# Optimization experiments

Measured on AMD Instinct MI355X. Metric: run time of the kernel, lower is better.

The kernel has to match this reference:

```python
import jax, jax.numpy as jnp
import numpy as np

B, C_HIGH, C_LOW, H, W = 4, 256, 128, 64, 64
HEADS = 4
HEAD_DIM = C_LOW // HEADS
FFN = 2 * C_LOW
EPS = 1e-5


def group_norm1(x, w, b):
    # GroupNorm(num_groups=1): normalize over (C,H,W) per sample, per-channel affine
    mu = jnp.mean(x, axis=(1, 2, 3), keepdims=True)
    var = jnp.var(x, axis=(1, 2, 3), keepdims=True)
    xn = (x - mu) * jax.lax.rsqrt(var + EPS)
    return xn * w[None, :, None, None] + b[None, :, None, None]


def conv1x1(x, Wm):
    # 1x1 conv, no bias: Wm [C_out, C_in], x [B,C_in,H,W]
    return jnp.einsum('oc,bchw->bohw', Wm, x)


def setup_inputs() -> dict:
    key = jax.random.key(0)
    ks = jax.random.split(key, 10)
    s = 0.05
    return {
        'high_feature': jax.random.normal(ks[0], (B, C_HIGH, H, W), jnp.float32),
        'low_feature': jax.random.normal(ks[1], (B, C_LOW, H, W), jnp.float32),
        'norm_high_w': jnp.ones((C_HIGH,), jnp.float32),
        'norm_high_b': jnp.zeros((C_HIGH,), jnp.float32),
        'norm_low_w': jnp.ones((C_LOW,), jnp.float32),
        'norm_low_b': jnp.zeros((C_LOW,), jnp.float32),
        'norm_ffn_w': jnp.ones((C_LOW,), jnp.float32),
        'norm_ffn_b': jnp.zeros((C_LOW,), jnp.float32),
        'Wq': jax.random.normal(ks[2], (C_LOW, C_HIGH), jnp.float32) * s,
        'Wk': jax.random.normal(ks[3], (C_LOW, C_LOW), jnp.float32) * s,
        'Wv': jax.random.normal(ks[4], (C_LOW, C_LOW), jnp.float32) * s,
        'Wproj': jax.random.normal(ks[5], (C_LOW, C_LOW), jnp.float32) * s,
        'Wffn1': jax.random.normal(ks[6], (FFN, C_LOW), jnp.float32) * s,
        'Wffn2': jax.random.normal(ks[7], (C_LOW, FFN), jnp.float32) * s,
        # nn.Parameter(torch.zeros(1)) in the original; use 0.1 for nontrivial grads
        'gamma_attn': jnp.full((1,), 0.1, jnp.float32),
        'gamma_ffn': jnp.full((1,), 0.1, jnp.float32),
    }


def reference(high_feature, low_feature, norm_high_w, norm_high_b, norm_low_w,
              norm_low_b, norm_ffn_w, norm_ffn_b, Wq, Wk, Wv, Wproj, Wffn1,
              Wffn2, gamma_attn, gamma_ffn):
    Bb, _, Hh, Ww = low_feature.shape
    N = Hh * Ww
    scale = HEAD_DIM ** (-0.5)

    high_norm = group_norm1(high_feature, norm_high_w, norm_high_b)
    low_norm = group_norm1(low_feature, norm_low_w, norm_low_b)

    q = conv1x1(high_norm, Wq).reshape(Bb, HEADS, HEAD_DIM, N).transpose(0, 1, 3, 2)  # [B,h,N,d]
    k = conv1x1(low_norm, Wk).reshape(Bb, HEADS, HEAD_DIM, N)                         # [B,h,d,N]
    v = conv1x1(low_norm, Wv).reshape(Bb, HEADS, HEAD_DIM, N).transpose(0, 1, 3, 2)   # [B,h,N,d]

    attn = jax.nn.softmax(jnp.einsum('bhnd,bhdm->bhnm', q, k) * scale, axis=-1)       # [B,h,N,N]
    out = jnp.einsum('bhnm,bhmd->bhnd', attn, v)                                      # [B,h,N,d]
    out = out.transpose(0, 1, 3, 2).reshape(Bb, C_LOW, Hh, Ww)
    out = conv1x1(out, Wproj)

    x = low_feature + gamma_attn[0] * out
    xn = group_norm1(x, norm_ffn_w, norm_ffn_b)
    ffn = conv1x1(jax.nn.gelu(conv1x1(xn, Wffn1), approximate=False), Wffn2)
    return x + gamma_ffn[0] * ffn
```

## Files before the change

kernel.cpp:

```cpp
#include <hip/hip_runtime.h>
#include <hip/hip_bf16.h>
#include <math.h>

#define EPS 1e-5f
#define BB 4
#define CHIGH 256
#define CLOW 128
#define NN 4096
#define NHEADS 4
#define HDIM 32
#define FFN_DIM 256
#define SPLITS 4

typedef __bf16 b8 __attribute__((ext_vector_type(8)));
typedef float f4 __attribute__((ext_vector_type(4)));

__device__ __forceinline__ unsigned int cvt_pk(float lo, float hi) {
    float2 t; t.x = lo; t.y = hi;
    __hip_bfloat162 h = __float22bfloat162_rn(t);
    unsigned int r;
    __builtin_memcpy(&r, &h, sizeof(r));
    return r;
}
__device__ __forceinline__ float b2f(unsigned short u) {
    unsigned int x = ((unsigned int)u) << 16;
    float f;
    __builtin_memcpy(&f, &x, 4);
    return f;
}
__device__ __forceinline__ float fexp2(float x) {
#if __has_builtin(__builtin_amdgcn_exp2f)
    return __builtin_amdgcn_exp2f(x);
#else
    return exp2f(x);
#endif
}

__global__ __launch_bounds__(256)
void prep_kernel(const float* __restrict__ high, const float* __restrict__ low,
                 float* __restrict__ acc,
                 const float* __restrict__ w0, const float* __restrict__ w1,
                 const float* __restrict__ w2, const float* __restrict__ w3,
                 const float* __restrict__ w4, const float* __restrict__ w5,
                 unsigned short* __restrict__ dst)
{
    const int z = blockIdx.z;
    if (z < 2) {
        const int perSample = z == 0 ? CHIGH * NN : CLOW * NN;
        const float* X = z == 0 ? high : low;
        float* ac = acc + (z == 0 ? 0 : 8);
        const int b = blockIdx.y;
        const float4* xp = (const float4*)(X + (size_t)b * perSample);
        const int n4 = perSample >> 2;
        float s = 0.f, s2 = 0.f;
        for (int i = blockIdx.x * blockDim.x + threadIdx.x; i < n4;
             i += gridDim.x * blockDim.x) {
            float4 v = xp[i];
            s  += v.x + v.y + v.z + v.w;
            s2 += v.x * v.x + v.y * v.y + v.z * v.z + v.w * v.w;
        }
        for (int off = 32; off; off >>= 1) {
            s  += __shfl_down(s, off, 64);
            s2 += __shfl_down(s2, off, 64);
        }
        __shared__ float ls[4], ls2[4];
        const int w = threadIdx.x >> 6;
        if ((threadIdx.x & 63) == 0) { ls[w] = s; ls2[w] = s2; }
        __syncthreads();
        if (threadIdx.x == 0) {
            atomicAdd(&ac[2 * b], ls[0] + ls[1] + ls[2] + ls[3]);
            atomicAdd(&ac[2 * b + 1], ls2[0] + ls2[1] + ls2[2] + ls2[3]);
        }
    } else {
        const int idx = blockIdx.y * 64 + blockIdx.x;
        const int m = idx >> 5;
        if (m >= 6) return;
        const int sizes[6] = {32768, 16384, 16384, 16384, 32768, 32768};
        const int offs[6]  = {0, 32768, 49152, 65536, 81920, 114688};
        const int Ks[6]    = {256, 128, 128, 128, 128, 256};
        const float* src = m == 0 ? w0 : m == 1 ? w1 : m == 2 ? w2 : m == 3 ? w3
                         : m == 4 ? w4 : w5;
        const int i = ((idx & 31) * 256 + threadIdx.x) * 4;
        if (i >= sizes[m]) return;
        const int K = Ks[m];
        const int row = i / K, col = i % K;
        const int mt = row >> 4, mr = row & 15;
        const int kt = col >> 5, kr = col & 31;
        float4 v = *(const float4*)&src[i];
        uint2 pk;
        pk.x = cvt_pk(v.x, v.y);
        pk.y = cvt_pk(v.z, v.w);
        const int doff = offs[m] + (((mt * (K >> 5)) + kt) << 9) + (mr << 5) + kr;
        *(uint2*)&dst[doff] = pk;
    }
}

__global__ __launch_bounds__(256)
void qkv_kernel(const unsigned short* __restrict__ wbf,
                const float* __restrict__ high, const float* __restrict__ low,
                unsigned short* __restrict__ Qt, unsigned short* __restrict__ Kt,
                unsigned short* __restrict__ Vt,
                const float* __restrict__ nh_w, const float* __restrict__ nh_b,
                const float* __restrict__ nl_w, const float* __restrict__ nl_b,
                const float* __restrict__ st)
{
    __shared__ unsigned short XsRaw[32 * 264];
    const int b = blockIdx.y;
    const int n0 = blockIdx.x * 32;
    const int t = threadIdx.x;
    const int w = t >> 6, lm = t & 15, quad = (t & 63) >> 4;
    const int fo = lm * 32 + quad * 8;
    unsigned int* xw = (unsigned int*)XsRaw;

    if (blockIdx.z == 0) {
        const float invCnt = 1.0f / ((float)CHIGH * NN);
        const float mean = st[2 * b] * invCnt;
        const float rstd = rsqrtf(st[2 * b + 1] * invCnt - mean * mean + EPS);
        const float* Xb = high + (size_t)b * CHIGH * NN;
        #pragma unroll
        for (int it = 0; it < 4; it++) {
            const int s = it * 256 + t;
            const int kp = s >> 3;
            const int k2 = kp << 1;
            const int nc = (s & 7) << 2;
            const size_t ro = (size_t)k2 * NN + n0 + nc;
            float4 pa = *(const float4*)&Xb[ro];
            float4 pb = *(const float4*)&Xb[ro + NN];
            const float sc0 = nh_w[k2] * rstd,     sb0 = nh_b[k2] - mean * sc0;
            const float sc1 = nh_w[k2 + 1] * rstd, sb1 = nh_b[k2 + 1] - mean * sc1;
            pa.x = pa.x * sc0 + sb0; pa.y = pa.y * sc0 + sb0;
            pa.z = pa.z * sc0 + sb0; pa.w = pa.w * sc0 + sb0;
            pb.x = pb.x * sc1 + sb1; pb.y = pb.y * sc1 + sb1;
            pb.z = pb.z * sc1 + sb1; pb.w = pb.w * sc1 + sb1;
            xw[(nc + 0) * 132 + kp] = cvt_pk(pa.x, pb.x);
            xw[(nc + 1) * 132 + kp] = cvt_pk(pa.y, pb.y);
            xw[(nc + 2) * 132 + kp] = cvt_pk(pa.z, pb.z);
            xw[(nc + 3) * 132 + kp] = cvt_pk(pa.w, pb.w);
        }
        __syncthreads();
        const int ng = w & 1, mh = w >> 1;
        f4 acc[4];
        #pragma unroll
        for (int f = 0; f < 4; f++) acc[f] = (f4){0.f, 0.f, 0.f, 0.f};
        #pragma unroll
        for (int kc = 0; kc < 8; kc++) {
            b8 bx = *(const b8*)&XsRaw[(ng * 16 + lm) * 264 + kc * 32 + quad * 8];
            #pragma unroll
            for (int f = 0; f < 4; f++) {
                b8 af = *(const b8*)&wbf[(((mh * 4 + f) * 8 + kc) << 9) + fo];
                acc[f] = __builtin_amdgcn_mfma_f32_16x16x32_bf16(af, bx, acc[f], 0, 0, 0);
            }
        }
        const int n = n0 + ng * 16 + lm;
        const float oscale = 0.25503480f;
        #pragma unroll
        for (int f = 0; f < 4; f++) {
            const int mb = mh * 64 + f * 16 + quad * 4;
            const int hh = mb >> 5, ddb = mb & 31;
            uint2 pk;
            pk.x = cvt_pk(acc[f][0] * oscale, acc[f][1] * oscale);
            pk.y = cvt_pk(acc[f][2] * oscale, acc[f][3] * oscale);
            *(uint2*)&Qt[((size_t)(b * NHEADS + hh) * NN + n) * 32 + ddb] = pk;
        }
    } else {
        const unsigned short* Wb = wbf + 32768;
        const float invCnt = 1.0f / ((float)CLOW * NN);
        const float mean = st[8 + 2 * b] * invCnt;
        const float rstd = rsqrtf(st[8 + 2 * b + 1] * invCnt - mean * mean + EPS);
        const float* Xb = low + (size_t)b * CLOW * NN;
        #pragma unroll
        for (int it = 0; it < 2; it++) {
            const int s = it * 256 + t;
            const int kp = s >> 3;
            const int k2 = kp << 1;
            const int nc = (s & 7) << 2;
            const size_t ro = (size_t)k2 * NN + n0 + nc;
            float4 pa = *(const float4*)&Xb[ro];
            float4 pb = *(const float4*)&Xb[ro + NN];
            const float sc0 = nl_w[k2] * rstd,     sb0 = nl_b[k2] - mean * sc0;
            const float sc1 = nl_w[k2 + 1] * rstd, sb1 = nl_b[k2 + 1] - mean * sc1;
            pa.x = pa.x * sc0 + sb0; pa.y = pa.y * sc0 + sb0;
            pa.z = pa.z * sc0 + sb0; pa.w = pa.w * sc0 + sb0;
            pb.x = pb.x * sc1 + sb1; pb.y = pb.y * sc1 + sb1;
            pb.z = pb.z * sc1 + sb1; pb.w = pb.w * sc1 + sb1;
            xw[(nc + 0) * 68 + kp] = cvt_pk(pa.x, pb.x);
            xw[(nc + 1) * 68 + kp] = cvt_pk(pa.y, pb.y);
            xw[(nc + 2) * 68 + kp] = cvt_pk(pa.z, pb.z);
            xw[(nc + 3) * 68 + kp] = cvt_pk(pa.w, pb.w);
        }
        __syncthreads();
        f4 acc[2][4];
        #pragma unroll
        for (int ng = 0; ng < 2; ng++)
            #pragma unroll
            for (int f = 0; f < 4; f++) acc[ng][f] = (f4){0.f, 0.f, 0.f, 0.f};
        #pragma unroll
        for (int kc = 0; kc < 4; kc++) {
            b8 bx0 = *(const b8*)&XsRaw[lm * 136 + kc * 32 + quad * 8];
            b8 bx1 = *(const b8*)&XsRaw[(16 + lm) * 136 + kc * 32 + quad * 8];
            #pragma unroll
            for (int f = 0; f < 4; f++) {
                b8 af = *(const b8*)&Wb[(((w * 4 + f) * 4 + kc) << 9) + fo];
                acc[0][f] = __builtin_amdgcn_mfma_f32_16x16x32_bf16(af, bx0, acc[0][f], 0, 0, 0);
                acc[1][f] = __builtin_amdgcn_mfma_f32_16x16x32_bf16(af, bx1, acc[1][f], 0, 0, 0);
            }
        }
        if (w < 2) {
            #pragma unroll
            for (int ng = 0; ng < 2; ng++) {
                const int n = n0 + ng * 16 + lm;
                #pragma unroll
                for (int f = 0; f < 4; f++) {
                    const int mb = w * 64 + f * 16 + quad * 4;
                    const int hh = mb >> 5, ddb = mb & 31;
                    uint2 pk;
                    pk.x = cvt_pk(acc[ng][f][0], acc[ng][f][1]);
                    pk.y = cvt_pk(acc[ng][f][2], acc[ng][f][3]);
                    *(uint2*)&Kt[((size_t)(b * NHEADS + hh) * NN + n) * 32 + ddb] = pk;
                }
            }
        } else {
            #pragma unroll
            for (int ng = 0; ng < 2; ng++) {
                const int n = n0 + ng * 16 + lm;
                const size_t nblk = ((size_t)(n >> 5) << 10) + (n & 31);
                #pragma unroll
                for (int f = 0; f < 4; f++) {
                    const int db = (w - 2) * 64 + f * 16 + quad * 4;
                    const int hh = db >> 5;
                    const size_t hb = (size_t)(b * NHEADS + hh) * NN * 32;
                    #pragma unroll
                    for (int r = 0; r < 4; r++) {
                        const int d = (db + r) & 31;
                        unsigned int u = cvt_pk(acc[ng][f][r], 0.f);
                        Vt[hb + nblk + (size_t)d * 32] = (unsigned short)(u & 0xFFFF);
                    }
                }
            }
        }
    }
}

__global__ __launch_bounds__(256)
void flash_kernel(const unsigned short* __restrict__ Qt,
                  const unsigned short* __restrict__ Kt,
                  const unsigned short* __restrict__ Vt,
                  unsigned short* __restrict__ Op, float* __restrict__ Lp)
{
    __shared__ unsigned short Ps[4][32][72];

    const int bz = blockIdx.z;
    const int b = bz >> 2, half = bz & 3;
    const int h = blockIdx.y;
    const int n0 = blockIdx.x * 128;
    const int t = threadIdx.x;
    const int w = t >> 6;
    const int lm = t & 15, quad = (t & 63) >> 4;

    const unsigned short* Qh = Qt + (size_t)(b * NHEADS + h) * NN * 32;
    const unsigned short* Kh = Kt + (size_t)(b * NHEADS + h) * NN * 32;
    const unsigned short* Vh = Vt + (size_t)(b * NHEADS + h) * NN * 32;

    b8 aq[2];
    aq[0] = *(const b8*)&Qh[(size_t)(n0 + w * 32 + lm) * 32 + quad * 8];
    aq[1] = *(const b8*)&Qh[(size_t)(n0 + w * 32 + 16 + lm) * 32 + quad * 8];

    b8 ones;
    #pragma unroll
    for (int j = 0; j < 8; j++) ones[j] = (__bf16)1.0f;

    f4 ocT[2][2];
    f4 lsum[2];
    #pragma unroll
    for (int u = 0; u < 2; u++) {
        lsum[u] = (f4){0.f, 0.f, 0.f, 0.f};
        ocT[0][u] = (f4){0.f, 0.f, 0.f, 0.f};
        ocT[1][u] = (f4){0.f, 0.f, 0.f, 0.f};
    }

    auto loadFrags = [&](int m0, b8* bk, b8 (*av)[2]) {
        #pragma unroll
        for (int f = 0; f < 4; f++)
            bk[f] = *(const b8*)&Kh[(size_t)(m0 + f * 16 + lm) * 32 + quad * 8];
        #pragma unroll
        for (int c = 0; c < 2; c++) {
            const size_t vb = (size_t)(m0 + c * 32) * 32 + quad * 8;
            av[0][c] = *(const b8*)&Vh[vb + (size_t)lm * 32];
            av[1][c] = *(const b8*)&Vh[vb + (size_t)(16 + lm) * 32];
        }
    };

    auto computeTile = [&](const b8* bk, const b8 (*av)[2]) {
        #pragma unroll
        for (int f = 0; f < 4; f++) {
            #pragma unroll
            for (int u = 0; u < 2; u++) {
                f4 z = {0.f, 0.f, 0.f, 0.f};
                f4 sv = __builtin_amdgcn_mfma_f32_16x16x32_bf16(bk[f], aq[u], z, 0, 0, 0);
                uint2 pk;
                pk.x = cvt_pk(fexp2(sv[0]), fexp2(sv[1]));
                pk.y = cvt_pk(fexp2(sv[2]), fexp2(sv[3]));
                *(uint2*)&Ps[w][u * 16 + lm][f * 16 + quad * 4] = pk;
            }
        }
        #pragma unroll
        for (int c = 0; c < 2; c++)
            #pragma unroll
            for (int u = 0; u < 2; u++) {
                b8 bp = *(const b8*)&Ps[w][u * 16 + lm][c * 32 + quad * 8];
                ocT[0][u] = __builtin_amdgcn_mfma_f32_16x16x32_bf16(av[0][c], bp, ocT[0][u], 0, 0, 0);
                ocT[1][u] = __builtin_amdgcn_mfma_f32_16x16x32_bf16(av[1][c], bp, ocT[1][u], 0, 0, 0);
                lsum[u]   = __builtin_amdgcn_mfma_f32_16x16x32_bf16(ones, bp, lsum[u], 0, 0, 0);
            }
    };

    const int m_lo = half * (NN / SPLITS);
    constexpr int nT = NN / SPLITS / 64;
    b8 bkA[4], bkB[4];
    b8 avA[2][2], avB[2][2];
    loadFrags(m_lo, bkA, avA);
    #pragma unroll 1
    for (int it = 0; it < nT; it += 2) {
        loadFrags(m_lo + (it + 1) * 64, bkB, avB);
        computeTile(bkA, avA);
        const int m0n = (it + 2 < nT) ? m_lo + (it + 2) * 64 : m_lo;
        loadFrags(m0n, bkA, avA);
        computeTile(bkB, avB);
    }

    unsigned short* OpB = Op + ((size_t)(half * BB + b) * CLOW + h * HDIM) * NN;
    float* LpB = Lp + ((size_t)(half * BB + b) * NHEADS + h) * NN;
    #pragma unroll
    for (int u = 0; u < 2; u++) {
        const int n = n0 + w * 32 + u * 16 + lm;
        if (quad == 0) LpB[n] = lsum[u][0];
        #pragma unroll
        for (int hh = 0; hh < 2; hh++)
            #pragma unroll
            for (int r = 0; r < 4; r++) {
                const int d = hh * 16 + quad * 4 + r;
                unsigned int uu = cvt_pk(ocT[hh][u][r], 0.f);
                OpB[(size_t)d * NN + n] = (unsigned short)(uu & 0xFFFF);
            }
    }
}

__global__ __launch_bounds__(256)
void proj_kernel(const unsigned short* __restrict__ Wb,
                 const unsigned short* __restrict__ Opart, const float* __restrict__ Lp,
                 const float* __restrict__ low, float* __restrict__ Xout,
                 const float* __restrict__ gp, float* __restrict__ stOut)
{
    __shared__ unsigned short Xs[32][136];
    __shared__ float red[8];
    const int b = blockIdx.z;
    const int mblk = blockIdx.y;
    const int n0 = blockIdx.x * 32;
    const int t = threadIdx.x;
    const int w = t >> 6, lm = t & 15, quad = (t & 63) >> 4;
    const int ng = w & 1, mh = w >> 1;
    const int fo = lm * 32 + quad * 8;
    unsigned int* xw = (unsigned int*)&Xs[0][0];

    #pragma unroll
    for (int it = 0; it < 2; it++) {
        const int s = it * 256 + t;
        const int kp = s >> 3;
        const int k2 = kp << 1;
        const int nc = (s & 7) << 2;
        const size_t ro = (size_t)k2 * NN + n0 + nc;
        const int hh = k2 >> 5;
        const size_t lo = (size_t)(b * NHEADS + hh) * NN + n0 + nc;
        float4 l4 = *(const float4*)&Lp[lo];
        #pragma unroll
        for (int sp = 1; sp < SPLITS; sp++)
            l4 += *(const float4*)&Lp[lo + (size_t)sp * BB * NHEADS * NN];
        float4 pa = {0.f, 0.f, 0.f, 0.f}, pb = {0.f, 0.f, 0.f, 0.f};
        #pragma unroll
        for (int sp = 0; sp < SPLITS; sp++) {
            const unsigned short* Os = Opart + (size_t)sp * BB * CLOW * NN
                                     + (size_t)b * CLOW * NN + ro;
            ushort4 ua = *(const ushort4*)Os;
            ushort4 ub = *(const ushort4*)(Os + NN);
            pa.x += b2f(ua.x); pa.y += b2f(ua.y); pa.z += b2f(ua.z); pa.w += b2f(ua.w);
            pb.x += b2f(ub.x); pb.y += b2f(ub.y); pb.z += b2f(ub.z); pb.w += b2f(ub.w);
        }
        float4 iv;
        iv.x = 1.f / l4.x; iv.y = 1.f / l4.y; iv.z = 1.f / l4.z; iv.w = 1.f / l4.w;
        pa.x *= iv.x; pa.y *= iv.y; pa.z *= iv.z; pa.w *= iv.w;
        pb.x *= iv.x; pb.y *= iv.y; pb.z *= iv.z; pb.w *= iv.w;
        xw[(nc + 0) * 68 + kp] = cvt_pk(pa.x, pb.x);
        xw[(nc + 1) * 68 + kp] = cvt_pk(pa.y, pb.y);
        xw[(nc + 2) * 68 + kp] = cvt_pk(pa.z, pb.z);
        xw[(nc + 3) * 68 + kp] = cvt_pk(pa.w, pb.w);
    }
    __syncthreads();

    f4 acc[2];
    acc[0] = (f4){0.f, 0.f, 0.f, 0.f};
    acc[1] = (f4){0.f, 0.f, 0.f, 0.f};
    #pragma unroll
    for (int kc = 0; kc < 4; kc++) {
        b8 bx = *(const b8*)&Xs[ng * 16 + lm][kc * 32 + quad * 8];
        #pragma unroll
        for (int f = 0; f < 2; f++) {
            const int mt = mblk * 4 + mh * 2 + f;
            b8 af = *(const b8*)&Wb[((mt * 4 + kc) << 9) + fo];
            acc[f] = __builtin_amdgcn_mfma_f32_16x16x32_bf16(af, bx, acc[f], 0, 0, 0);
        }
    }

    const float g = gp[0];
    const float* Rb = low + (size_t)b * CLOW * NN;
    float* Yb = Xout + (size_t)b * CLOW * NN;
    const int n = n0 + ng * 16 + lm;
    float s = 0.f, s2 = 0.f;
    #pragma unroll
    for (int f = 0; f < 2; f++)
        #pragma unroll
        for (int r = 0; r < 4; r++) {
            const int m = mblk * 64 + mh * 32 + f * 16 + quad * 4 + r;
            const size_t off = (size_t)m * NN + n;
            float v = Rb[off] + g * acc[f][r];
            Yb[off] = v;
            s += v; s2 += v * v;
        }
    for (int off = 32; off; off >>= 1) {
        s  += __shfl_down(s, off, 64);
        s2 += __shfl_down(s2, off, 64);
    }
    if ((t & 63) == 0) { red[w] = s; red[4 + w] = s2; }
    __syncthreads();
    if (t == 0) {
        atomicAdd(&stOut[2 * b], red[0] + red[1] + red[2] + red[3]);
        atomicAdd(&stOut[2 * b + 1], red[4] + red[5] + red[6] + red[7]);
    }
}

__global__ __launch_bounds__(512)
void ffn_kernel(const unsigned short* __restrict__ W1, const unsigned short* __restrict__ W2,
                const float* __restrict__ X, float* __restrict__ Out,
                const float* __restrict__ nw, const float* __restrict__ nb,
                const float* __restrict__ st, const float* __restrict__ gp)
{
    __shared__ unsigned short Xs[32][136];
    __shared__ unsigned short Hs[32][264];
    const int b = blockIdx.y;
    const int n0 = blockIdx.x * 32;
    const int t = threadIdx.x;
    const int w = t >> 6, lm = t & 15, quad = (t & 63) >> 4;
    const int fo = lm * 32 + quad * 8;

    const float invCnt = 1.0f / ((float)CLOW * NN);
    const float mean = st[2 * b] * invCnt;
    const float rstd = rsqrtf(st[2 * b + 1] * invCnt - mean * mean + EPS);

    const float* Xb = X + (size_t)b * CLOW * NN;
    unsigned int* xw = (unsigned int*)&Xs[0][0];
    {
        const int s = t;
        const int kp = s >> 3;
        const int k2 = kp << 1;
        const int nc = (s & 7) << 2;
        const size_t ro = (size_t)k2 * NN + n0 + nc;
        float4 pa = *(const float4*)&Xb[ro];
        float4 pb = *(const float4*)&Xb[ro + NN];
        const float sc0 = nw[k2] * rstd,     sb0 = nb[k2] - mean * sc0;
        const float sc1 = nw[k2 + 1] * rstd, sb1 = nb[k2 + 1] - mean * sc1;
        pa.x = pa.x * sc0 + sb0; pa.y = pa.y * sc0 + sb0;
        pa.z = pa.z * sc0 + sb0; pa.w = pa.w * sc0 + sb0;
        pb.x = pb.x * sc1 + sb1; pb.y = pb.y * sc1 + sb1;
        pb.z = pb.z * sc1 + sb1; pb.w = pb.w * sc1 + sb1;
        xw[(nc + 0) * 68 + kp] = cvt_pk(pa.x, pb.x);
        xw[(nc + 1) * 68 + kp] = cvt_pk(pa.y, pb.y);
        xw[(nc + 2) * 68 + kp] = cvt_pk(pa.z, pb.z);
        xw[(nc + 3) * 68 + kp] = cvt_pk(pa.w, pb.w);
    }
    __syncthreads();

    f4 hv[2][2];
    #pragma unroll
    for (int ng = 0; ng < 2; ng++) {
        hv[ng][0] = (f4){0.f, 0.f, 0.f, 0.f};
        hv[ng][1] = (f4){0.f, 0.f, 0.f, 0.f};
    }
    #pragma unroll
    for (int kc = 0; kc < 4; kc++) {
        b8 bx0 = *(const b8*)&Xs[lm][kc * 32 + quad * 8];
        b8 bx1 = *(const b8*)&Xs[16 + lm][kc * 32 + quad * 8];
        #pragma unroll
        for (int f = 0; f < 2; f++) {
            const int mt = w * 2 + f;
            b8 af = *(const b8*)&W1[((mt * 4 + kc) << 9) + fo];
            hv[0][f] = __builtin_amdgcn_mfma_f32_16x16x32_bf16(af, bx0, hv[0][f], 0, 0, 0);
            hv[1][f] = __builtin_amdgcn_mfma_f32_16x16x32_bf16(af, bx1, hv[1][f], 0, 0, 0);
        }
    }
    #pragma unroll
    for (int ng = 0; ng < 2; ng++)
        #pragma unroll
        for (int f = 0; f < 2; f++) {
            float g0 = hv[ng][f][0], g1 = hv[ng][f][1];
            float g2 = hv[ng][f][2], g3 = hv[ng][f][3];
            g0 = 0.5f * g0 * (1.f + erff(g0 * 0.70710678118654752f));
            g1 = 0.5f * g1 * (1.f + erff(g1 * 0.70710678118654752f));
            g2 = 0.5f * g2 * (1.f + erff(g2 * 0.70710678118654752f));
            g3 = 0.5f * g3 * (1.f + erff(g3 * 0.70710678118654752f));
            uint2 pk;
            pk.x = cvt_pk(g0, g1);
            pk.y = cvt_pk(g2, g3);
            *(uint2*)&Hs[ng * 16 + lm][w * 32 + f * 16 + quad * 4] = pk;
        }
    __syncthreads();

    f4 o[2];
    o[0] = (f4){0.f, 0.f, 0.f, 0.f};
    o[1] = (f4){0.f, 0.f, 0.f, 0.f};
    #pragma unroll
    for (int kc = 0; kc < 8; kc++) {
        b8 bh0 = *(const b8*)&Hs[lm][kc * 32 + quad * 8];
        b8 bh1 = *(const b8*)&Hs[16 + lm][kc * 32 + quad * 8];
        b8 af = *(const b8*)&W2[((w * 8 + kc) << 9) + fo];
        o[0] = __builtin_amdgcn_mfma_f32_16x16x32_bf16(af, bh0, o[0], 0, 0, 0);
        o[1] = __builtin_amdgcn_mfma_f32_16x16x32_bf16(af, bh1, o[1], 0, 0, 0);
    }
    const float g = gp[0];
    float* Ob = Out + (size_t)b * CLOW * NN;
    #pragma unroll
    for (int ng = 0; ng < 2; ng++) {
        const int n = n0 + ng * 16 + lm;
        #pragma unroll
        for (int r = 0; r < 4; r++) {
            const int m = w * 16 + quad * 4 + r;
            const size_t off = (size_t)m * NN + n;
            Ob[off] = Xb[off] + g * o[ng][r];
        }
    }
}

extern "C" void kernel_launch(void* const* d_in, const int* in_sizes, int n_in,
                              void* d_out, int out_size, void* d_ws, size_t ws_size,
                              hipStream_t stream)
{
    const float* high  = (const float*)d_in[0];
    const float* low   = (const float*)d_in[1];
    const float* nh_w  = (const float*)d_in[2];
    const float* nh_b  = (const float*)d_in[3];
    const float* nl_w  = (const float*)d_in[4];
    const float* nl_b  = (const float*)d_in[5];
    const float* nf_w  = (const float*)d_in[6];
    const float* nf_b  = (const float*)d_in[7];
    const float* Wq    = (const float*)d_in[8];
    const float* Wk    = (const float*)d_in[9];
    const float* Wv    = (const float*)d_in[10];
    const float* Wproj = (const float*)d_in[11];
    const float* Wff1  = (const float*)d_in[12];
    const float* Wff2  = (const float*)d_in[13];
    const float* g_at  = (const float*)d_in[14];
    const float* g_ff  = (const float*)d_in[15];
    float* out = (float*)d_out;

    float* ws    = (float*)d_ws;
    float* stats = ws;
    unsigned short* wbf = (unsigned short*)(ws + 64);
    unsigned short* qt = wbf + 147456;
    unsigned short* kt = qt + (size_t)BB * NHEADS * NN * 32;
    unsigned short* vt = kt + (size_t)BB * NHEADS * NN * 32;
    unsigned short* opart = vt + (size_t)BB * CLOW * NN;
    float* lpart = (float*)(opart + (size_t)SPLITS * BB * CLOW * NN);
    float* x     = lpart + (size_t)SPLITS * BB * NHEADS * NN;

    (void)hipMemsetAsync(stats, 0, 64 * sizeof(float), stream);

    prep_kernel<<<dim3(64, BB, 3), 256, 0, stream>>>(high, low, stats,
                                                     Wq, Wk, Wv, Wproj, Wff1, Wff2, wbf);

    qkv_kernel<<<dim3(128, BB, 2), 256, 0, stream>>>(wbf, high, low, qt, kt, vt,
                                                     nh_w, nh_b, nl_w, nl_b, stats);

    flash_kernel<<<dim3(NN / 128, NHEADS, BB * SPLITS), 256, 0, stream>>>(qt, kt, vt,
                                                                          opart, lpart);

    proj_kernel<<<dim3(128, 2, BB), 256, 0, stream>>>(wbf + 65536, opart, lpart,
                                                      low, x, g_at, stats + 16);

    ffn_kernel<<<dim3(128, BB), 512, 0, stream>>>(wbf + 81920, wbf + 114688, x, out,
                                                  nf_w, nf_b, stats + 16, g_ff);
}
```

Measured before the change: 236.6 us.

## Remap flash blocks per XCD and widen blocks to eight waves

Swaps the 3D grid of the attention kernel for a 1D grid of 1024 blocks of 512 threads. Block indices are remapped so each XCD handles a contiguous set of (split, batch, head) groups, which keeps K/V reuse inside one XCD's L2. The manual double-buffered K/V register prefetch is removed in favour of a simple loop, and the S computation is split into separate MFMA, exp and store phases. In exchange, the compiler's scheduler now has to hide load latency, and the larger blocks raise register pressure.

```diff
diff --git a/kernel.cpp b/kernel.cpp
--- a/kernel.cpp
+++ b/kernel.cpp
@@ -241,18 +241,21 @@
     }
 }
 
-__global__ __launch_bounds__(256)
+__global__ __launch_bounds__(512)
 void flash_kernel(const unsigned short* __restrict__ Qt,
                   const unsigned short* __restrict__ Kt,
                   const unsigned short* __restrict__ Vt,
                   unsigned short* __restrict__ Op, float* __restrict__ Lp)
 {
-    __shared__ unsigned short Ps[4][32][72];
-
-    const int bz = blockIdx.z;
-    const int b = bz >> 2, half = bz & 3;
-    const int h = blockIdx.y;
-    const int n0 = blockIdx.x * 128;
+    __shared__ unsigned short Ps[8][32][72];
+
+    const int lid = blockIdx.x;
+    const int xcd = lid & 7, slot = lid >> 3;
+    const int g = xcd * 8 + (slot >> 4);
+    const int xblk = slot & 15;
+    const int half = g >> 4, bh = g & 15;
+    const int b = bh >> 2, h = bh & 3;
+    const int n0 = xblk * 256;
     const int t = threadIdx.x;
     const int w = t >> 6;
     const int lm = t & 15, quad = (t & 63) >> 4;
@@ -278,7 +281,9 @@
         ocT[1][u] = (f4){0.f, 0.f, 0.f, 0.f};
     }
 
-    auto loadFrags = [&](int m0, b8* bk, b8 (*av)[2]) {
+    const int m_lo = half * (NN / SPLITS), m_hi = m_lo + NN / SPLITS;
+    for (int m0 = m_lo; m0 < m_hi; m0 += 64) {
+        b8 bk[4], av[2][2];
         #pragma unroll
         for (int f = 0; f < 4; f++)
             bk[f] = *(const b8*)&Kh[(size_t)(m0 + f * 16 + lm) * 32 + quad * 8];
@@ -288,21 +293,26 @@
             av[0][c] = *(const b8*)&Vh[vb + (size_t)lm * 32];
             av[1][c] = *(const b8*)&Vh[vb + (size_t)(16 + lm) * 32];
         }
-    };
-
-    auto computeTile = [&](const b8* bk, const b8 (*av)[2]) {
-        #pragma unroll
-        for (int f = 0; f < 4; f++) {
+
+        f4 st[4][2];
+        #pragma unroll
+        for (int f = 0; f < 4; f++)
             #pragma unroll
             for (int u = 0; u < 2; u++) {
                 f4 z = {0.f, 0.f, 0.f, 0.f};
-                f4 sv = __builtin_amdgcn_mfma_f32_16x16x32_bf16(bk[f], aq[u], z, 0, 0, 0);
+                st[f][u] = __builtin_amdgcn_mfma_f32_16x16x32_bf16(bk[f], aq[u], z, 0, 0, 0);
+            }
+
+        #pragma unroll
+        for (int f = 0; f < 4; f++)
+            #pragma unroll
+            for (int u = 0; u < 2; u++) {
                 uint2 pk;
-                pk.x = cvt_pk(fexp2(sv[0]), fexp2(sv[1]));
-                pk.y = cvt_pk(fexp2(sv[2]), fexp2(sv[3]));
+                pk.x = cvt_pk(fexp2(st[f][u][0]), fexp2(st[f][u][1]));
+                pk.y = cvt_pk(fexp2(st[f][u][2]), fexp2(st[f][u][3]));
                 *(uint2*)&Ps[w][u * 16 + lm][f * 16 + quad * 4] = pk;
             }
-        }
+
         #pragma unroll
         for (int c = 0; c < 2; c++)
             #pragma unroll
@@ -312,20 +322,6 @@
                 ocT[1][u] = __builtin_amdgcn_mfma_f32_16x16x32_bf16(av[1][c], bp, ocT[1][u], 0, 0, 0);
                 lsum[u]   = __builtin_amdgcn_mfma_f32_16x16x32_bf16(ones, bp, lsum[u], 0, 0, 0);
             }
-    };
-
-    const int m_lo = half * (NN / SPLITS);
-    constexpr int nT = NN / SPLITS / 64;
-    b8 bkA[4], bkB[4];
-    b8 avA[2][2], avB[2][2];
-    loadFrags(m_lo, bkA, avA);
-    #pragma unroll 1
-    for (int it = 0; it < nT; it += 2) {
-        loadFrags(m_lo + (it + 1) * 64, bkB, avB);
-        computeTile(bkA, avA);
-        const int m0n = (it + 2 < nT) ? m_lo + (it + 2) * 64 : m_lo;
-        loadFrags(m0n, bkA, avA);
-        computeTile(bkB, avB);
     }
 
     unsigned short* OpB = Op + ((size_t)(half * BB + b) * CLOW + h * HDIM) * NN;
@@ -578,8 +574,7 @@
     qkv_kernel<<<dim3(128, BB, 2), 256, 0, stream>>>(wbf, high, low, qt, kt, vt,
                                                      nh_w, nh_b, nl_w, nl_b, stats);
 
-    flash_kernel<<<dim3(NN / 128, NHEADS, BB * SPLITS), 256, 0, stream>>>(qt, kt, vt,
-                                                                          opart, lpart);
+    flash_kernel<<<dim3(1024), 512, 0, stream>>>(qt, kt, vt, opart, lpart);
 
     proj_kernel<<<dim3(128, 2, BB), 256, 0, stream>>>(wbf + 65536, opart, lpart,
                                                       low, x, g_at, stats + 16);
```

Result: faster. 229.7 us (-2.9%).
